# Kernel optimization log

Hardware: AMD Instinct MI355X
Metric: run time of the kernel (lower is better)

## Reference

```python
import jax, jax.numpy as jnp
import numpy as np

B, C_EDGE, C_FUSED, C_SEM = 4, 64, 128, 128
H = W = 64
MASK_SIZE = 11
EPS = 1e-6


def _window_mask(h, w, mask_size):
    # M_dw: 0 inside the clipped (mask_size x mask_size) window around each query pixel, -10000 outside.
    half = mask_size // 2
    idx = jnp.arange(h * w)
    qx, qy = idx // w, idx % w
    inside = (jnp.abs(qx[:, None] - qx[None, :]) <= half) & (jnp.abs(qy[:, None] - qy[None, :]) <= half)
    return jnp.where(inside, 0.0, -10000.0).astype(jnp.float32)


def _conv1x1(x, w, b):
    # x: [b, cin, h, w], w: [cout, cin]
    return jnp.einsum('bchw,oc->bohw', x, w) + b[None, :, None, None]


def _proj1d(x, w, b):
    # x: [b, cin, n], w: [cout, cin]
    return jnp.einsum('bcn,oc->bon', x, w) + b[None, :, None]


def _bilinear(x, h, w):
    # matches F.interpolate(mode='bilinear', align_corners=False)
    b, c = x.shape[0], x.shape[1]
    return jax.image.resize(x, (b, c, h, w), method='linear', antialias=False)


def setup_inputs() -> dict:
    key = jax.random.key(0)
    ks = jax.random.split(key, 13)
    s = 0.05
    return {
        'edge_features': jax.random.normal(ks[0], (B, C_EDGE, 32, 32), jnp.float32),
        'semantic_features': jax.random.normal(ks[1], (B, C_SEM, H, W), jnp.float32),
        'fused_features': jax.random.normal(ks[2], (B, C_FUSED, 32, 32), jnp.float32),
        'w_align': jax.random.normal(ks[3], (C_SEM, C_EDGE), jnp.float32) * s,
        'b_align': jax.random.normal(ks[4], (C_SEM,), jnp.float32) * s,
        'w_fused_align': jax.random.normal(ks[5], (C_SEM, C_FUSED), jnp.float32) * s,
        'b_fused_align': jax.random.normal(ks[6], (C_SEM,), jnp.float32) * s,
        'w_q': jax.random.normal(ks[7], (2 * C_SEM, 2 * C_SEM), jnp.float32) * s,
        'b_q': jax.random.normal(ks[8], (2 * C_SEM,), jnp.float32) * s,
        'w_k': jax.random.normal(ks[9], (2 * C_SEM, 2 * C_SEM), jnp.float32) * s,
        'b_k': jax.random.normal(ks[10], (2 * C_SEM,), jnp.float32) * s,
        'w_fusion': jax.random.normal(ks[11], (C_SEM, 2 * C_SEM), jnp.float32) * s,
        'b_fusion': jax.random.normal(ks[12], (C_SEM,), jnp.float32) * s,
    }


def reference(edge_features, semantic_features, fused_features,
              w_align, b_align, w_fused_align, b_fused_align,
              w_q, b_q, w_k, b_k, w_fusion, b_fusion):
    b, c, h, w = semantic_features.shape
    n = h * w

    edge = _conv1x1(_bilinear(edge_features, h, w), w_align, b_align)            # [b,c,h,w]
    fused = _conv1x1(_bilinear(fused_features, h, w), w_fused_align, b_fused_align)

    l2_edge = jnp.sqrt(jnp.sum(edge * edge, axis=1, keepdims=True))              # [b,1,h,w]
    l2_sem = jnp.sqrt(jnp.sum(semantic_features * semantic_features, axis=1, keepdims=True))
    similarity = jnp.sum((edge / (l2_edge + EPS)) * (semantic_features / (l2_sem + EPS)),
                         axis=1, keepdims=True)
    similarity = (similarity + 1.0) * 0.5

    density_flat = l2_edge.reshape(b, n)
    density = (jax.nn.softmax(density_flat, axis=1) * n).reshape(b, 1, h, w)

    edge_t = (edge * similarity).reshape(b, c, n)
    sem_t = (semantic_features * density).reshape(b, c, n)
    fused_t = fused.reshape(b, c, n)
    sem_raw = semantic_features.reshape(b, c, n)

    edge_cat = jnp.concatenate([edge_t, edge_t], axis=1)    # [b,2c,n]
    sem_cat = jnp.concatenate([sem_t, fused_t], axis=1)
    sem_val = jnp.concatenate([sem_raw, fused_t], axis=1)

    q = _proj1d(edge_cat, w_q, b_q)                          # [b,2c,n]
    k = _proj1d(sem_cat, w_k, b_k)

    scale = 1.0 / jnp.sqrt(jnp.float32(2 * c))
    attn = jnp.einsum('bcn,bcm->bnm', q, k) * scale          # [b,n,n]
    attn = attn + _window_mask(h, w, MASK_SIZE)
    attn = jax.nn.softmax(attn, axis=-1)

    out = jnp.einsum('bnm,bcm->bnc', attn, sem_val)          # [b,n,2c]
    out = out.reshape(b, h, w, 2 * c).transpose(0, 3, 1, 2)  # [b,2c,h,w]
    return _conv1x1(out, w_fusion, b_fusion)
```

## Files before the change

kernel.cpp:

```cpp
#include <hip/hip_runtime.h>
#include <hip/hip_bf16.h>

#define NB 4
#define C 128
#define N 4096
#define EPS 1e-6f
#define PW 80
#define PIMG 5120

typedef float f32x4 __attribute__((ext_vector_type(4)));
typedef short bf16x8 __attribute__((ext_vector_type(8)));
typedef unsigned short ushort_t;
typedef unsigned int uint_t;

__device__ __forceinline__ ushort_t f2bf(float f) {
  __hip_bfloat16 h = __float2bfloat16(f);
  return *reinterpret_cast<ushort_t*>(&h);
}

struct alignas(8) us4 { ushort_t a, b, c, d; };

__device__ __forceinline__ void conv_body(const float* __restrict__ x,
                                          const float* __restrict__ w,
                                          const float* __restrict__ bias,
                                          float* __restrict__ out,
                                          int n, int o0, int b, int CIN) {
  const float* xb = x + (size_t)(b * CIN) * 1024 + n;
  float a0 = 0.f, a1 = 0.f, a2 = 0.f, a3 = 0.f;
  for (int c = 0; c < CIN; ++c) {
    float xv = xb[(size_t)c * 1024];
    a0 += w[(o0 + 0) * CIN + c] * xv;
    a1 += w[(o0 + 1) * CIN + c] * xv;
    a2 += w[(o0 + 2) * CIN + c] * xv;
    a3 += w[(o0 + 3) * CIN + c] * xv;
  }
  size_t ob = ((size_t)b * 128 + o0) * 1024 + n;
  out[ob]        = a0 + bias[o0];
  out[ob + 1024] = a1 + bias[o0 + 1];
  out[ob + 2048] = a2 + bias[o0 + 2];
  out[ob + 3072] = a3 + bias[o0 + 3];
}

__global__ void prep_misc(const float* __restrict__ edge_f, const float* __restrict__ w_align,
                          const float* __restrict__ b_align,
                          const float* __restrict__ fused_f, const float* __restrict__ w_fal,
                          const float* __restrict__ b_fal,
                          const float* __restrict__ wq, const float* __restrict__ wk,
                          const float* __restrict__ wf,
                          ushort_t* __restrict__ wqf, ushort_t* __restrict__ wkf,
                          ushort_t* __restrict__ wff,
                          float* __restrict__ edge32, float* __restrict__ fused32,
                          float* __restrict__ dsum) {
  int bx = blockIdx.x, t = threadIdx.x;
  if (bx < 64) {
    if (bx == 0 && t < NB) dsum[t] = 0.f;
    int c = bx * 256 + t;
    int lane = c & 63;
    int mrow = lane & 15, quad = lane >> 4;
    if (c < 4096) {
      int grp = c >> 6;
      int tile = grp >> 2, kslot = grp & 3;
      int o = tile * 16 + mrow, k0 = kslot * 32 + quad * 8;
      const float* s = wq + o * 256 + k0;
      ushort_t* d = wqf + (size_t)c * 8;
#pragma unroll
      for (int j = 0; j < 8; ++j) d[j] = f2bf(s[j] + s[128 + j]);
    } else if (c < 12288) {
      int c2 = c - 4096;
      int grp = c2 >> 6;
      int tile = grp >> 3, kslot = grp & 7;
      int o = tile * 16 + mrow, k0 = kslot * 32 + quad * 8;
      const float* s = wk + o * 256 + k0;
      ushort_t* d = wkf + (size_t)c2 * 8;
#pragma unroll
      for (int j = 0; j < 8; ++j) d[j] = f2bf(s[j]);
    } else {
      int c2 = c - 12288;
      int grp = c2 >> 6;
      int tile = grp >> 3, kslot = grp & 7;
      int o = tile * 16 + mrow, k0 = kslot * 32 + quad * 8;
      const float* s = wf + o * 256 + k0;
      ushort_t* d = wff + (size_t)c2 * 8;
#pragma unroll
      for (int j = 0; j < 8; ++j) d[j] = f2bf(s[j]);
    }
  } else if (bx < 576) {
    int j = bx - 64;
    conv_body(edge_f, w_align, b_align, edge32, (j & 3) * 256 + t, ((j >> 2) & 31) * 4, j >> 7, 64);
  } else {
    int j = bx - 576;
    conv_body(fused_f, w_fal, b_fal, fused32, (j & 3) * 256 + t, ((j >> 2) & 31) * 4, j >> 7, 128);
  }
}

__global__ __launch_bounds__(512, 4) void prep_acts(const float* __restrict__ edge32,
                                                    const float* __restrict__ fused32,
                                                    const float* __restrict__ sem,
                                                    const ushort_t* __restrict__ wqf,
                                                    const ushort_t* __restrict__ wff,
                                                    const float* __restrict__ b_q,
                                                    ushort_t* __restrict__ xt_sem,
                                                    ushort_t* __restrict__ xt_fused,
                                                    float* __restrict__ simb,
                                                    float* __restrict__ l2e,
                                                    float* __restrict__ dsum,
                                                    ushort_t* __restrict__ qtb,
                                                    ushort_t* __restrict__ v2b) {
  int b = blockIdx.y, bx = blockIdx.x;
  int y = bx >> 1, xh = (bx & 1) * 32;
  int t = threadIdx.x;
  int nl = t & 31, cg = t >> 5;
  int x = xh + nl;
  int yy0 = (y & 1) ? (y >> 1) : (y >> 1) - 1;
  float fy = (y & 1) ? 0.25f : 0.75f;
  int y0c = max(yy0, 0), y1c = min(yy0 + 1, 31);
  int xx0 = (x & 1) ? (x >> 1) : (x >> 1) - 1;
  float fx = (x & 1) ? 0.25f : 0.75f;
  int x0c = max(xx0, 0), x1c = min(xx0 + 1, 31);

  __shared__ uint_t se[32][68], ssm[32][68], sf[32][68];
  __shared__ float red[8][3][32];
  __shared__ float simL[32];
  __shared__ ushort_t vstg[128 * 40];

  float ee = 0.f, ssum = 0.f, es = 0.f;
#pragma unroll 2
  for (int p = 0; p < 4; ++p) {
    float evs[2], fvs[2], svs[2];
#pragma unroll
    for (int u = 0; u < 2; ++u) {
      int c = cg * 8 + p * 2 + u;
      const float* ip = edge32 + ((size_t)(b * 128 + c)) * 1024;
      float e00 = ip[y0c * 32 + x0c], e01 = ip[y0c * 32 + x1c];
      float e10 = ip[y1c * 32 + x0c], e11 = ip[y1c * 32 + x1c];
      float ev = (1.f - fy) * ((1.f - fx) * e00 + fx * e01) + fy * ((1.f - fx) * e10 + fx * e11);
      const float* fp = fused32 + ((size_t)(b * 128 + c)) * 1024;
      float f00 = fp[y0c * 32 + x0c], f01 = fp[y0c * 32 + x1c];
      float f10 = fp[y1c * 32 + x0c], f11 = fp[y1c * 32 + x1c];
      float fv = (1.f - fy) * ((1.f - fx) * f00 + fx * f01) + fy * ((1.f - fx) * f10 + fx * f11);
      float sv = sem[((size_t)(b * 128 + c)) * 4096 + y * 64 + x];
      ee += ev * ev; ssum += sv * sv; es += ev * sv;
      evs[u] = ev; fvs[u] = fv; svs[u] = sv;
    }
    int col = cg * 4 + p;
    se[nl][col]  = (uint_t)f2bf(evs[0]) | ((uint_t)f2bf(evs[1]) << 16);
    sf[nl][col]  = (uint_t)f2bf(fvs[0]) | ((uint_t)f2bf(fvs[1]) << 16);
    ssm[nl][col] = (uint_t)f2bf(svs[0]) | ((uint_t)f2bf(svs[1]) << 16);
  }
  ee += __shfl_xor(ee, 32, 64); ssum += __shfl_xor(ssum, 32, 64); es += __shfl_xor(es, 32, 64);
  int w = t >> 6, lane = t & 63;
  int l15 = lane & 15, quad = lane >> 4;
  if (lane < 32) { red[w][0][lane] = ee; red[w][1][lane] = ssum; red[w][2][lane] = es; }
  __syncthreads();

  int base_n = b * 4096 + y * 64 + xh;
#pragma unroll
  for (int rep = 0; rep < 4; ++rep) {
    int d = rep * 512 + t;
    int r = d >> 6, cp = d & 63;
    ((uint_t*)xt_sem)[(size_t)(base_n + r) * 64 + cp] = ssm[r][cp];
    ((uint_t*)xt_fused)[(size_t)(base_n + r) * 64 + cp] = sf[r][cp];
  }
  if (t < 32) {
    float E = 0.f, S = 0.f, X = 0.f;
#pragma unroll
    for (int w2 = 0; w2 < 8; ++w2) { E += red[w2][0][t]; S += red[w2][1][t]; X += red[w2][2][t]; }
    float le = sqrtf(E), ls = sqrtf(S);
    float sv = (X / ((le + EPS) * (ls + EPS)) + 1.f) * 0.5f;
    simb[base_n + t] = sv;
    simL[t] = sv;
    l2e[base_n + t] = le;
    float pe = expf(le - 16.f);
#pragma unroll
    for (int m2 = 16; m2; m2 >>= 1) pe += __shfl_xor(pe, m2, 64);
    if (t == 0) atomicAdd(&dsum[b], pe);
  }
  __syncthreads();

#pragma unroll
  for (int h = 0; h < 2; ++h) {
    f32x4 vacc = (f32x4){0.f,0.f,0.f,0.f};
#pragma unroll
    for (int kk = 0; kk < 4; ++kk) {
      bf16x8 bfr = *(const bf16x8*)&ssm[h * 16 + l15][kk * 16 + quad * 4];
      bf16x8 afr = *(const bf16x8*)(wff + (size_t)((w * 8 + kk) * 64 + lane) * 8);
      vacc = __builtin_amdgcn_mfma_f32_16x16x32_bf16(afr, bfr, vacc, 0, 0, 0);
    }
#pragma unroll
    for (int kk = 0; kk < 4; ++kk) {
      bf16x8 bfr = *(const bf16x8*)&sf[h * 16 + l15][kk * 16 + quad * 4];
      bf16x8 afr = *(const bf16x8*)(wff + (size_t)((w * 8 + 4 + kk) * 64 + lane) * 8);
      vacc = __builtin_amdgcn_mfma_f32_16x16x32_bf16(afr, bfr, vacc, 0, 0, 0);
    }
#pragma unroll
    for (int r = 0; r < 4; ++r) {
      int ch = w * 16 + quad * 4 + r;
      vstg[ch * 40 + h * 16 + l15] = f2bf(vacc[r]);
    }
  }

#pragma unroll
  for (int h = 0; h < 2; ++h) {
    f32x4 qacc[2];
#pragma unroll
    for (int i = 0; i < 2; ++i) qacc[i] = (f32x4){0.f,0.f,0.f,0.f};
#pragma unroll
    for (int kk = 0; kk < 4; ++kk) {
      bf16x8 bfr = *(const bf16x8*)&se[h * 16 + l15][kk * 16 + quad * 4];
#pragma unroll
      for (int i = 0; i < 2; ++i) {
        bf16x8 afr = *(const bf16x8*)(wqf + (size_t)(((w * 2 + i) * 4 + kk) * 64 + lane) * 8);
        qacc[i] = __builtin_amdgcn_mfma_f32_16x16x32_bf16(afr, bfr, qacc[i], 0, 0, 0);
      }
    }
    int px = h * 16 + l15;
    float sv = simL[px];
    int n = y * 64 + xh + px;
#pragma unroll
    for (int i = 0; i < 2; ++i) {
      int o = (w * 2 + i) * 16 + quad * 4;
      float4 bq = *(const float4*)(b_q + o);
      us4 pk = { f2bf(sv * qacc[i][0] + bq.x), f2bf(sv * qacc[i][1] + bq.y),
                 f2bf(sv * qacc[i][2] + bq.z), f2bf(sv * qacc[i][3] + bq.w) };
      *(us4*)(qtb + ((size_t)b * N + n) * 256 + o) = pk;
    }
  }

  __syncthreads();
  int np0 = y * PW + 8 + xh;
  {
    int ch = t >> 2, seg = t & 3;
    *(bf16x8*)(v2b + ((size_t)b * 128 + ch) * PIMG + np0 + seg * 8) =
        *(const bf16x8*)&vstg[ch * 40 + seg * 8];
  }
}

__global__ __launch_bounds__(256, 4) void gemm_k(const ushort_t* __restrict__ xt_sem,
                                                 const ushort_t* __restrict__ xt_fused,
                                                 const ushort_t* __restrict__ wkf,
                                                 const float* __restrict__ b_k,
                                                 const float* __restrict__ l2e,
                                                 const float* __restrict__ dsum,
                                                 ushort_t* __restrict__ ktb) {
  int bx = blockIdx.x, bI = blockIdx.y;
  int t = threadIdx.x, w = t >> 6, lane = t & 63;
  int mrow = lane & 15, quad = lane >> 4;
  __shared__ __align__(16) ushort_t stg[16 * 264];

  int n0 = bx * 16, o0 = w * 64;
  float dscale = 4096.f / dsum[bI];
  const ushort_t* bS = xt_sem + ((size_t)bI * N + n0 + mrow) * 128 + quad * 8;
  const ushort_t* bF = xt_fused + ((size_t)bI * N + n0 + mrow) * 128 + quad * 8;
  f32x4 accL[4], accR[4];
#pragma unroll
  for (int i = 0; i < 4; ++i) { accL[i] = (f32x4){0.f,0.f,0.f,0.f}; accR[i] = (f32x4){0.f,0.f,0.f,0.f}; }
#pragma unroll
  for (int kk = 0; kk < 4; ++kk) {
    bf16x8 bfr = *(const bf16x8*)(bS + kk * 32);
#pragma unroll
    for (int i = 0; i < 4; ++i) {
      bf16x8 afr = *(const bf16x8*)(wkf + (size_t)((((w * 4 + i) * 8) + kk) * 64 + lane) * 8);
      accL[i] = __builtin_amdgcn_mfma_f32_16x16x32_bf16(afr, bfr, accL[i], 0, 0, 0);
    }
  }
#pragma unroll
  for (int kk = 0; kk < 4; ++kk) {
    bf16x8 bfr = *(const bf16x8*)(bF + kk * 32);
#pragma unroll
    for (int i = 0; i < 4; ++i) {
      bf16x8 afr = *(const bf16x8*)(wkf + (size_t)((((w * 4 + i) * 8) + 4 + kk) * 64 + lane) * 8);
      accR[i] = __builtin_amdgcn_mfma_f32_16x16x32_bf16(afr, bfr, accR[i], 0, 0, 0);
    }
  }
  int n = n0 + mrow;
  float dv = expf(l2e[bI * N + n] - 16.f) * dscale;
#pragma unroll
  for (int i = 0; i < 4; ++i) {
    int o = o0 + i * 16 + quad * 4;
    float4 bk = *(const float4*)(b_k + o);
    us4 pk = { f2bf(accL[i][0] * dv + accR[i][0] + bk.x),
               f2bf(accL[i][1] * dv + accR[i][1] + bk.y),
               f2bf(accL[i][2] * dv + accR[i][2] + bk.z),
               f2bf(accL[i][3] * dv + accR[i][3] + bk.w) };
    *(us4*)&stg[mrow * 264 + o] = pk;
  }
  __syncthreads();
  int np0 = (n0 >> 6) * PW + 8 + (n0 & 63);
#pragma unroll
  for (int r = 0; r < 2; ++r) {
    int cidx = r * 256 + t;
    int row = cidx >> 5, cc = cidx & 31;
    *(bf16x8*)(ktb + ((size_t)bI * PIMG + np0 + row) * 256 + cc * 8) =
        *(const bf16x8*)&stg[row * 264 + cc * 8];
  }
}

__global__ __launch_bounds__(256) void attn_kernel(const ushort_t* __restrict__ qtb,
                                                   const ushort_t* __restrict__ ktb,
                                                   const ushort_t* __restrict__ v2b,
                                                   const float* __restrict__ b_fusion,
                                                   float* __restrict__ out) {
  int L = blockIdx.x;
  int xcd = L & 7, j = L >> 3;
  int b = xcd >> 1;
  int ty0 = (((xcd & 1) << 3) + (j >> 3)) * 4;
  int tx0 = (j & 7) * 8;
  int y0 = max(ty0 - 5, 0), y1 = min(ty0 + 8, 63);
  int nh = y1 - y0 + 1;
  int x0a = tx0 - 8, cb = tx0;
  int ntq = (nh * 3 + 1) >> 1;
  int npv = (nh * 3 + 3) >> 2;

  __shared__ ushort_t pst[32][352];
  __shared__ float redm[4][2][16], reds[4][2][16];

  int t = threadIdx.x, w = t >> 6, lane = t & 63;
  int l15 = lane & 15, quad = lane >> 4;

  int gap = npv * 32 - ntq * 16;
  for (int idx = t; idx < 32 * gap; idx += 256)
    pst[idx & 31][ntq * 16 + (idx >> 5)] = 0;

  int n_s0 = (ty0 + (l15 >> 3)) * 64 + tx0 + (l15 & 7);
  int n_s1 = n_s0 + 128;
  bf16x8 qfr[2][8];
  {
    const ushort_t* q0 = qtb + ((size_t)b * N + n_s0) * 256 + quad * 8;
    const ushort_t* q1 = qtb + ((size_t)b * N + n_s1) * 256 + quad * 8;
#pragma unroll
    for (int ks = 0; ks < 8; ++ks) {
      qfr[0][ks] = *(const bf16x8*)(q0 + ks * 32);
      qfr[1][ks] = *(const bf16x8*)(q1 + ks * 32);
    }
  }
  int qx = tx0 + (l15 & 7);
  int qy0 = ty0 + (l15 >> 3);

  const ushort_t* kb = ktb + (size_t)b * PIMG * 256;
  f32x4 sc[6][2];
#pragma unroll
  for (int i = 0; i < 6; ++i) {
    int tq = w + i * 4;
    if (tq >= ntq) break;
    int key = tq * 16 + l15;
    int ry = (key * 2731) >> 16;
    int rx = key - ry * 24;
    int yy = min(y0 + ry, 63);
    const ushort_t* krow = kb + (size_t)(yy * PW + cb + rx) * 256 + quad * 8;
    f32x4 a0 = (f32x4){0.f,0.f,0.f,0.f}, a1 = (f32x4){0.f,0.f,0.f,0.f};
#pragma unroll
    for (int ks = 0; ks < 8; ++ks) {
      bf16x8 afr = *(const bf16x8*)(krow + ks * 32);
      a0 = __builtin_amdgcn_mfma_f32_16x16x32_bf16(afr, qfr[0][ks], a0, 0, 0, 0);
      a1 = __builtin_amdgcn_mfma_f32_16x16x32_bf16(afr, qfr[1][ks], a1, 0, 0, 0);
    }
    sc[i][0] = a0; sc[i][1] = a1;
  }
  float mymax0 = -1e30f, mymax1 = -1e30f;
#pragma unroll
  for (int i = 0; i < 6; ++i) {
    int tq = w + i * 4;
    if (tq >= ntq) break;
#pragma unroll
    for (int r = 0; r < 4; ++r) {
      int key = tq * 16 + quad * 4 + r;
      int ry = (key * 2731) >> 16;
      int rx = key - ry * 24;
      int x = x0a + rx;
      int dx = x - qx;
      bool xok = (dx >= -5) && (dx <= 5) && (x >= 0) && (x <= 63) && (ry < nh);
      int dy0 = y0 + ry - qy0;
      float s0 = (xok && dy0 >= -5 && dy0 <= 5) ? sc[i][0][r] * 0.0625f : -1e30f;
      int dy1 = dy0 - 2;
      float s1 = (xok && dy1 >= -5 && dy1 <= 5) ? sc[i][1][r] * 0.0625f : -1e30f;
      sc[i][0][r] = s0; sc[i][1][r] = s1;
      mymax0 = fmaxf(mymax0, s0); mymax1 = fmaxf(mymax1, s1);
    }
  }
  mymax0 = fmaxf(mymax0, __shfl_xor(mymax0, 16, 64));
  mymax0 = fmaxf(mymax0, __shfl_xor(mymax0, 32, 64));
  mymax1 = fmaxf(mymax1, __shfl_xor(mymax1, 16, 64));
  mymax1 = fmaxf(mymax1, __shfl_xor(mymax1, 32, 64));
  if (quad == 0) { redm[w][0][l15] = mymax0; redm[w][1][l15] = mymax1; }
  __syncthreads();
  float gmax0 = fmaxf(fmaxf(redm[0][0][l15], redm[1][0][l15]), fmaxf(redm[2][0][l15], redm[3][0][l15]));
  float gmax1 = fmaxf(fmaxf(redm[0][1][l15], redm[1][1][l15]), fmaxf(redm[2][1][l15], redm[3][1][l15]));
  float mysum0 = 0.f, mysum1 = 0.f;
#pragma unroll
  for (int i = 0; i < 6; ++i) {
    int tq = w + i * 4;
    if (tq >= ntq) break;
#pragma unroll
    for (int r = 0; r < 4; ++r) {
      float e0 = expf(sc[i][0][r] - gmax0);
      float e1 = expf(sc[i][1][r] - gmax1);
      sc[i][0][r] = e0; sc[i][1][r] = e1;
      mysum0 += e0; mysum1 += e1;
    }
  }
  mysum0 += __shfl_xor(mysum0, 16, 64); mysum0 += __shfl_xor(mysum0, 32, 64);
  mysum1 += __shfl_xor(mysum1, 16, 64); mysum1 += __shfl_xor(mysum1, 32, 64);
  if (quad == 0) { reds[w][0][l15] = mysum0; reds[w][1][l15] = mysum1; }
#pragma unroll
  for (int i = 0; i < 6; ++i) {
    int tq = w + i * 4;
    if (tq >= ntq) break;
    int kc = tq * 16 + quad * 4;
#pragma unroll
    for (int s = 0; s < 2; ++s) {
      uint_t p01 = (uint_t)f2bf(sc[i][s][0]) | ((uint_t)f2bf(sc[i][s][1]) << 16);
      uint_t p23 = (uint_t)f2bf(sc[i][s][2]) | ((uint_t)f2bf(sc[i][s][3]) << 16);
      *(uint_t*)(&pst[s * 16 + l15][kc]) = p01;
      *(uint_t*)(&pst[s * 16 + l15][kc + 2]) = p23;
    }
  }
  __syncthreads();

  float rinv0 = 1.f / (reds[0][0][l15] + reds[1][0][l15] + reds[2][0][l15] + reds[3][0][l15]);
  float rinv1 = 1.f / (reds[0][1][l15] + reds[1][1][l15] + reds[2][1][l15] + reds[3][1][l15]);

  const ushort_t* vb = v2b + (size_t)b * 128 * PIMG;
#pragma unroll
  for (int half = 0; half < 2; ++half) {
    int ch0 = half * 64 + w * 16;
    const ushort_t* vrow = vb + (size_t)(ch0 + l15) * PIMG;
    f32x4 acc0 = (f32x4){0.f,0.f,0.f,0.f}, acc1 = (f32x4){0.f,0.f,0.f,0.f};
    for (int ks = 0; ks < npv; ++ks) {
      int kst = ks * 32 + quad * 8;
      int ry = (kst * 2731) >> 16;
      int rxs = kst - ry * 24;
      int yy = min(y0 + ry, 63);
      bf16x8 av = *(const bf16x8*)(vrow + yy * PW + cb + rxs);
      bf16x8 bp0 = *(const bf16x8*)(&pst[l15][kst]);
      bf16x8 bp1 = *(const bf16x8*)(&pst[16 + l15][kst]);
      acc0 = __builtin_amdgcn_mfma_f32_16x16x32_bf16(av, bp0, acc0, 0, 0, 0);
      acc1 = __builtin_amdgcn_mfma_f32_16x16x32_bf16(av, bp1, acc1, 0, 0, 0);
    }
    int chg = ch0 + quad * 4;
    float4 bf4 = *(const float4*)(b_fusion + chg);
    float bfa[4] = {bf4.x, bf4.y, bf4.z, bf4.w};
#pragma unroll
    for (int r = 0; r < 4; ++r) {
      out[((size_t)b * 128 + chg + r) * N + n_s0] = acc0[r] * rinv0 + bfa[r];
      out[((size_t)b * 128 + chg + r) * N + n_s1] = acc1[r] * rinv1 + bfa[r];
    }
  }
}

extern "C" void kernel_launch(void* const* d_in, const int* in_sizes, int n_in,
                              void* d_out, int out_size, void* d_ws, size_t ws_size,
                              hipStream_t stream) {
  (void)in_sizes; (void)n_in; (void)out_size; (void)ws_size;
  const float* edge_f  = (const float*)d_in[0];
  const float* sem     = (const float*)d_in[1];
  const float* fused_f = (const float*)d_in[2];
  const float* w_align = (const float*)d_in[3];
  const float* b_align = (const float*)d_in[4];
  const float* w_fal   = (const float*)d_in[5];
  const float* b_fal   = (const float*)d_in[6];
  const float* w_q     = (const float*)d_in[7];
  const float* b_q     = (const float*)d_in[8];
  const float* w_k     = (const float*)d_in[9];
  const float* b_k     = (const float*)d_in[10];
  const float* w_fus   = (const float*)d_in[11];
  const float* b_fus   = (const float*)d_in[12];
  float* out = (float*)d_out;

  float* ws = (float*)d_ws;
  float* edge32   = ws;
  float* fused32  = ws + 524288;
  float* simb     = ws + 1048576;
  float* l2e      = ws + 1064960;
  float* dsum     = ws + 1081344;
  ushort_t* xt_sem   = (ushort_t*)(ws + 1097728);
  ushort_t* xt_fused = (ushort_t*)(ws + 2146304);
  ushort_t* wqf      = (ushort_t*)(ws + 3194880);
  ushort_t* wkf      = (ushort_t*)(ws + 3211264);
  ushort_t* wff      = (ushort_t*)(ws + 3244032);
  ushort_t* qtb      = (ushort_t*)(ws + 3260416);
  ushort_t* ktb      = (ushort_t*)(ws + 5357568);
  ushort_t* v2b      = (ushort_t*)(ws + 7979008);

  prep_misc<<<1088, 256, 0, stream>>>(edge_f, w_align, b_align, fused_f, w_fal, b_fal,
                                      w_q, w_k, w_fus, wqf, wkf, wff, edge32, fused32, dsum);
  prep_acts<<<dim3(128, NB), 512, 0, stream>>>(edge32, fused32, sem, wqf, wff, b_q,
                                               xt_sem, xt_fused, simb, l2e, dsum, qtb, v2b);
  gemm_k<<<dim3(256, NB), 256, 0, stream>>>(xt_sem, xt_fused, wkf, b_k, l2e, dsum, ktb);
  attn_kernel<<<512, 256, 0, stream>>>(qtb, ktb, v2b, b_fus, out);
}
```

Baseline: 159.6 us.

## Fuse K projection into prep_acts via cooperative grid sync

```diff
diff --git a/kernel.cpp b/kernel.cpp
--- a/kernel.cpp
+++ b/kernel.cpp
@@ -1,5 +1,8 @@
 #include <hip/hip_runtime.h>
 #include <hip/hip_bf16.h>
+#include <hip/hip_cooperative_groups.h>
+
+namespace cgrp = cooperative_groups;
 
 #define NB 4
 #define C 128
@@ -93,205 +96,192 @@
   }
 }
 
-__global__ __launch_bounds__(512, 4) void prep_acts(const float* __restrict__ edge32,
+__global__ __launch_bounds__(512, 2) void prep_acts(const float* __restrict__ edge32,
                                                     const float* __restrict__ fused32,
                                                     const float* __restrict__ sem,
                                                     const ushort_t* __restrict__ wqf,
+                                                    const ushort_t* __restrict__ wkf,
                                                     const ushort_t* __restrict__ wff,
                                                     const float* __restrict__ b_q,
-                                                    ushort_t* __restrict__ xt_sem,
-                                                    ushort_t* __restrict__ xt_fused,
-                                                    float* __restrict__ simb,
-                                                    float* __restrict__ l2e,
+                                                    const float* __restrict__ b_k,
                                                     float* __restrict__ dsum,
                                                     ushort_t* __restrict__ qtb,
+                                                    ushort_t* __restrict__ ktb,
                                                     ushort_t* __restrict__ v2b) {
-  int b = blockIdx.y, bx = blockIdx.x;
-  int y = bx >> 1, xh = (bx & 1) * 32;
+  __shared__ uint_t se[2][32][68], ssm[2][32][68], sf[2][32][68];
+  __shared__ float red[8][3][32];
+  __shared__ float simL[2][32], l2eL[2][32];
+  __shared__ ushort_t vstg[128 * 40];
+  __shared__ __align__(16) ushort_t kstg[32 * 264];
+
   int t = threadIdx.x;
-  int nl = t & 31, cg = t >> 5;
-  int x = xh + nl;
-  int yy0 = (y & 1) ? (y >> 1) : (y >> 1) - 1;
-  float fy = (y & 1) ? 0.25f : 0.75f;
-  int y0c = max(yy0, 0), y1c = min(yy0 + 1, 31);
-  int xx0 = (x & 1) ? (x >> 1) : (x >> 1) - 1;
-  float fx = (x & 1) ? 0.25f : 0.75f;
-  int x0c = max(xx0, 0), x1c = min(xx0 + 1, 31);
-
-  __shared__ uint_t se[32][68], ssm[32][68], sf[32][68];
-  __shared__ float red[8][3][32];
-  __shared__ float simL[32];
-  __shared__ ushort_t vstg[128 * 40];
-
-  float ee = 0.f, ssum = 0.f, es = 0.f;
-#pragma unroll 2
-  for (int p = 0; p < 4; ++p) {
-    float evs[2], fvs[2], svs[2];
-#pragma unroll
-    for (int u = 0; u < 2; ++u) {
-      int c = cg * 8 + p * 2 + u;
-      const float* ip = edge32 + ((size_t)(b * 128 + c)) * 1024;
-      float e00 = ip[y0c * 32 + x0c], e01 = ip[y0c * 32 + x1c];
-      float e10 = ip[y1c * 32 + x0c], e11 = ip[y1c * 32 + x1c];
-      float ev = (1.f - fy) * ((1.f - fx) * e00 + fx * e01) + fy * ((1.f - fx) * e10 + fx * e11);
-      const float* fp = fused32 + ((size_t)(b * 128 + c)) * 1024;
-      float f00 = fp[y0c * 32 + x0c], f01 = fp[y0c * 32 + x1c];
-      float f10 = fp[y1c * 32 + x0c], f11 = fp[y1c * 32 + x1c];
-      float fv = (1.f - fy) * ((1.f - fx) * f00 + fx * f01) + fy * ((1.f - fx) * f10 + fx * f11);
-      float sv = sem[((size_t)(b * 128 + c)) * 4096 + y * 64 + x];
-      ee += ev * ev; ssum += sv * sv; es += ev * sv;
-      evs[u] = ev; fvs[u] = fv; svs[u] = sv;
-    }
-    int col = cg * 4 + p;
-    se[nl][col]  = (uint_t)f2bf(evs[0]) | ((uint_t)f2bf(evs[1]) << 16);
-    sf[nl][col]  = (uint_t)f2bf(fvs[0]) | ((uint_t)f2bf(fvs[1]) << 16);
-    ssm[nl][col] = (uint_t)f2bf(svs[0]) | ((uint_t)f2bf(svs[1]) << 16);
-  }
-  ee += __shfl_xor(ee, 32, 64); ssum += __shfl_xor(ssum, 32, 64); es += __shfl_xor(es, 32, 64);
+  int nl = t & 31, cgi = t >> 5;
   int w = t >> 6, lane = t & 63;
   int l15 = lane & 15, quad = lane >> 4;
-  if (lane < 32) { red[w][0][lane] = ee; red[w][1][lane] = ssum; red[w][2][lane] = es; }
-  __syncthreads();
-
-  int base_n = b * 4096 + y * 64 + xh;
-#pragma unroll
-  for (int rep = 0; rep < 4; ++rep) {
-    int d = rep * 512 + t;
-    int r = d >> 6, cp = d & 63;
-    ((uint_t*)xt_sem)[(size_t)(base_n + r) * 64 + cp] = ssm[r][cp];
-    ((uint_t*)xt_fused)[(size_t)(base_n + r) * 64 + cp] = sf[r][cp];
-  }
-  if (t < 32) {
-    float E = 0.f, S = 0.f, X = 0.f;
-#pragma unroll
-    for (int w2 = 0; w2 < 8; ++w2) { E += red[w2][0][t]; S += red[w2][1][t]; X += red[w2][2][t]; }
-    float le = sqrtf(E), ls = sqrtf(S);
-    float sv = (X / ((le + EPS) * (ls + EPS)) + 1.f) * 0.5f;
-    simb[base_n + t] = sv;
-    simL[t] = sv;
-    l2e[base_n + t] = le;
-    float pe = expf(le - 16.f);
-#pragma unroll
-    for (int m2 = 16; m2; m2 >>= 1) pe += __shfl_xor(pe, m2, 64);
-    if (t == 0) atomicAdd(&dsum[b], pe);
-  }
-  __syncthreads();
-
-#pragma unroll
-  for (int h = 0; h < 2; ++h) {
-    f32x4 vacc = (f32x4){0.f,0.f,0.f,0.f};
-#pragma unroll
-    for (int kk = 0; kk < 4; ++kk) {
-      bf16x8 bfr = *(const bf16x8*)&ssm[h * 16 + l15][kk * 16 + quad * 4];
-      bf16x8 afr = *(const bf16x8*)(wff + (size_t)((w * 8 + kk) * 64 + lane) * 8);
-      vacc = __builtin_amdgcn_mfma_f32_16x16x32_bf16(afr, bfr, vacc, 0, 0, 0);
-    }
-#pragma unroll
-    for (int kk = 0; kk < 4; ++kk) {
-      bf16x8 bfr = *(const bf16x8*)&sf[h * 16 + l15][kk * 16 + quad * 4];
-      bf16x8 afr = *(const bf16x8*)(wff + (size_t)((w * 8 + 4 + kk) * 64 + lane) * 8);
-      vacc = __builtin_amdgcn_mfma_f32_16x16x32_bf16(afr, bfr, vacc, 0, 0, 0);
-    }
-#pragma unroll
-    for (int r = 0; r < 4; ++r) {
-      int ch = w * 16 + quad * 4 + r;
-      vstg[ch * 40 + h * 16 + l15] = f2bf(vacc[r]);
-    }
-  }
-
-#pragma unroll
-  for (int h = 0; h < 2; ++h) {
-    f32x4 qacc[2];
-#pragma unroll
-    for (int i = 0; i < 2; ++i) qacc[i] = (f32x4){0.f,0.f,0.f,0.f};
-#pragma unroll
-    for (int kk = 0; kk < 4; ++kk) {
-      bf16x8 bfr = *(const bf16x8*)&se[h * 16 + l15][kk * 16 + quad * 4];
+
+  for (int u = 0; u < 2; ++u) {
+    int L = (int)blockIdx.x + u * 256;
+    int b = L >> 7, bxu = L & 127;
+    int y = bxu >> 1, xh = (bxu & 1) * 32;
+    int x = xh + nl;
+    int yy0 = (y & 1) ? (y >> 1) : (y >> 1) - 1;
+    float fy = (y & 1) ? 0.25f : 0.75f;
+    int y0c = max(yy0, 0), y1c = min(yy0 + 1, 31);
+    int xx0 = (x & 1) ? (x >> 1) : (x >> 1) - 1;
+    float fx = (x & 1) ? 0.25f : 0.75f;
+    int x0c = max(xx0, 0), x1c = min(xx0 + 1, 31);
+
+    float ee = 0.f, ssum = 0.f, es = 0.f;
+#pragma unroll 2
+    for (int p = 0; p < 4; ++p) {
+      float evs[2], fvs[2], svs[2];
+#pragma unroll
+      for (int uu = 0; uu < 2; ++uu) {
+        int c = cgi * 8 + p * 2 + uu;
+        const float* ip = edge32 + ((size_t)(b * 128 + c)) * 1024;
+        float e00 = ip[y0c * 32 + x0c], e01 = ip[y0c * 32 + x1c];
+        float e10 = ip[y1c * 32 + x0c], e11 = ip[y1c * 32 + x1c];
+        float ev = (1.f - fy) * ((1.f - fx) * e00 + fx * e01) + fy * ((1.f - fx) * e10 + fx * e11);
+        const float* fp = fused32 + ((size_t)(b * 128 + c)) * 1024;
+        float f00 = fp[y0c * 32 + x0c], f01 = fp[y0c * 32 + x1c];
+        float f10 = fp[y1c * 32 + x0c], f11 = fp[y1c * 32 + x1c];
+        float fv = (1.f - fy) * ((1.f - fx) * f00 + fx * f01) + fy * ((1.f - fx) * f10 + fx * f11);
+        float sv = sem[((size_t)(b * 128 + c)) * 4096 + y * 64 + x];
+        ee += ev * ev; ssum += sv * sv; es += ev * sv;
+        evs[uu] = ev; fvs[uu] = fv; svs[uu] = sv;
+      }
+      int col = cgi * 4 + p;
+      se[u][nl][col]  = (uint_t)f2bf(evs[0]) | ((uint_t)f2bf(evs[1]) << 16);
+      sf[u][nl][col]  = (uint_t)f2bf(fvs[0]) | ((uint_t)f2bf(fvs[1]) << 16);
+      ssm[u][nl][col] = (uint_t)f2bf(svs[0]) | ((uint_t)f2bf(svs[1]) << 16);
+    }
+    ee += __shfl_xor(ee, 32, 64); ssum += __shfl_xor(ssum, 32, 64); es += __shfl_xor(es, 32, 64);
+    if (lane < 32) { red[w][0][lane] = ee; red[w][1][lane] = ssum; red[w][2][lane] = es; }
+    __syncthreads();
+    if (t < 32) {
+      float E = 0.f, S = 0.f, X = 0.f;
+#pragma unroll
+      for (int w2 = 0; w2 < 8; ++w2) { E += red[w2][0][t]; S += red[w2][1][t]; X += red[w2][2][t]; }
+      float le = sqrtf(E), ls = sqrtf(S);
+      float sv = (X / ((le + EPS) * (ls + EPS)) + 1.f) * 0.5f;
+      simL[u][t] = sv;
+      l2eL[u][t] = le;
+      float pe = expf(le - 16.f);
+#pragma unroll
+      for (int m2 = 16; m2; m2 >>= 1) pe += __shfl_xor(pe, m2, 64);
+      if (t == 0) atomicAdd(&dsum[b], pe);
+    }
+    __syncthreads();
+  }
+
+  cgrp::this_grid().sync();
+
+  for (int u = 0; u < 2; ++u) {
+    int L = (int)blockIdx.x + u * 256;
+    int b = L >> 7, bxu = L & 127;
+    int y = bxu >> 1, xh = (bxu & 1) * 32;
+    int np0 = y * PW + 8 + xh;
+    float dscale = 4096.f / __hip_atomic_load(&dsum[b], __ATOMIC_RELAXED, __HIP_MEMORY_SCOPE_AGENT);
+
+#pragma unroll
+    for (int h = 0; h < 2; ++h) {
+      f32x4 vacc = (f32x4){0.f,0.f,0.f,0.f};
+#pragma unroll
+      for (int kk = 0; kk < 4; ++kk) {
+        bf16x8 bfr = *(const bf16x8*)&ssm[u][h * 16 + l15][kk * 16 + quad * 4];
+        bf16x8 afr = *(const bf16x8*)(wff + (size_t)((w * 8 + kk) * 64 + lane) * 8);
+        vacc = __builtin_amdgcn_mfma_f32_16x16x32_bf16(afr, bfr, vacc, 0, 0, 0);
+      }
+#pragma unroll
+      for (int kk = 0; kk < 4; ++kk) {
+        bf16x8 bfr = *(const bf16x8*)&sf[u][h * 16 + l15][kk * 16 + quad * 4];
+        bf16x8 afr = *(const bf16x8*)(wff + (size_t)((w * 8 + 4 + kk) * 64 + lane) * 8);
+        vacc = __builtin_amdgcn_mfma_f32_16x16x32_bf16(afr, bfr, vacc, 0, 0, 0);
+      }
+#pragma unroll
+      for (int r = 0; r < 4; ++r) {
+        int ch = w * 16 + quad * 4 + r;
+        vstg[ch * 40 + h * 16 + l15] = f2bf(vacc[r]);
+      }
+    }
+    __syncthreads();
+    {
+      int ch = t >> 2, seg = t & 3;
+      *(bf16x8*)(v2b + ((size_t)b * 128 + ch) * PIMG + np0 + seg * 8) =
+          *(const bf16x8*)&vstg[ch * 40 + seg * 8];
+    }
+
+#pragma unroll
+    for (int h = 0; h < 2; ++h) {
+      f32x4 aL[2], aR[2];
+#pragma unroll
+      for (int i = 0; i < 2; ++i) { aL[i] = (f32x4){0.f,0.f,0.f,0.f}; aR[i] = (f32x4){0.f,0.f,0.f,0.f}; }
+#pragma unroll
+      for (int kk = 0; kk < 4; ++kk) {
+        bf16x8 bfr = *(const bf16x8*)&ssm[u][h * 16 + l15][kk * 16 + quad * 4];
+#pragma unroll
+        for (int i = 0; i < 2; ++i) {
+          bf16x8 afr = *(const bf16x8*)(wkf + (size_t)((((w * 2 + i) * 8) + kk) * 64 + lane) * 8);
+          aL[i] = __builtin_amdgcn_mfma_f32_16x16x32_bf16(afr, bfr, aL[i], 0, 0, 0);
+        }
+      }
+#pragma unroll
+      for (int kk = 0; kk < 4; ++kk) {
+        bf16x8 bfr = *(const bf16x8*)&sf[u][h * 16 + l15][kk * 16 + quad * 4];
+#pragma unroll
+        for (int i = 0; i < 2; ++i) {
+          bf16x8 afr = *(const bf16x8*)(wkf + (size_t)((((w * 2 + i) * 8) + 4 + kk) * 64 + lane) * 8);
+          aR[i] = __builtin_amdgcn_mfma_f32_16x16x32_bf16(afr, bfr, aR[i], 0, 0, 0);
+        }
+      }
+      float dv = expf(l2eL[u][h * 16 + l15] - 16.f) * dscale;
 #pragma unroll
       for (int i = 0; i < 2; ++i) {
-        bf16x8 afr = *(const bf16x8*)(wqf + (size_t)(((w * 2 + i) * 4 + kk) * 64 + lane) * 8);
-        qacc[i] = __builtin_amdgcn_mfma_f32_16x16x32_bf16(afr, bfr, qacc[i], 0, 0, 0);
-      }
-    }
-    int px = h * 16 + l15;
-    float sv = simL[px];
-    int n = y * 64 + xh + px;
-#pragma unroll
-    for (int i = 0; i < 2; ++i) {
-      int o = (w * 2 + i) * 16 + quad * 4;
-      float4 bq = *(const float4*)(b_q + o);
-      us4 pk = { f2bf(sv * qacc[i][0] + bq.x), f2bf(sv * qacc[i][1] + bq.y),
-                 f2bf(sv * qacc[i][2] + bq.z), f2bf(sv * qacc[i][3] + bq.w) };
-      *(us4*)(qtb + ((size_t)b * N + n) * 256 + o) = pk;
-    }
-  }
-
-  __syncthreads();
-  int np0 = y * PW + 8 + xh;
-  {
-    int ch = t >> 2, seg = t & 3;
-    *(bf16x8*)(v2b + ((size_t)b * 128 + ch) * PIMG + np0 + seg * 8) =
-        *(const bf16x8*)&vstg[ch * 40 + seg * 8];
-  }
-}
-
-__global__ __launch_bounds__(256, 4) void gemm_k(const ushort_t* __restrict__ xt_sem,
-                                                 const ushort_t* __restrict__ xt_fused,
-                                                 const ushort_t* __restrict__ wkf,
-                                                 const float* __restrict__ b_k,
-                                                 const float* __restrict__ l2e,
-                                                 const float* __restrict__ dsum,
-                                                 ushort_t* __restrict__ ktb) {
-  int bx = blockIdx.x, bI = blockIdx.y;
-  int t = threadIdx.x, w = t >> 6, lane = t & 63;
-  int mrow = lane & 15, quad = lane >> 4;
-  __shared__ __align__(16) ushort_t stg[16 * 264];
-
-  int n0 = bx * 16, o0 = w * 64;
-  float dscale = 4096.f / dsum[bI];
-  const ushort_t* bS = xt_sem + ((size_t)bI * N + n0 + mrow) * 128 + quad * 8;
-  const ushort_t* bF = xt_fused + ((size_t)bI * N + n0 + mrow) * 128 + quad * 8;
-  f32x4 accL[4], accR[4];
-#pragma unroll
-  for (int i = 0; i < 4; ++i) { accL[i] = (f32x4){0.f,0.f,0.f,0.f}; accR[i] = (f32x4){0.f,0.f,0.f,0.f}; }
-#pragma unroll
-  for (int kk = 0; kk < 4; ++kk) {
-    bf16x8 bfr = *(const bf16x8*)(bS + kk * 32);
-#pragma unroll
-    for (int i = 0; i < 4; ++i) {
-      bf16x8 afr = *(const bf16x8*)(wkf + (size_t)((((w * 4 + i) * 8) + kk) * 64 + lane) * 8);
-      accL[i] = __builtin_amdgcn_mfma_f32_16x16x32_bf16(afr, bfr, accL[i], 0, 0, 0);
-    }
-  }
-#pragma unroll
-  for (int kk = 0; kk < 4; ++kk) {
-    bf16x8 bfr = *(const bf16x8*)(bF + kk * 32);
-#pragma unroll
-    for (int i = 0; i < 4; ++i) {
-      bf16x8 afr = *(const bf16x8*)(wkf + (size_t)((((w * 4 + i) * 8) + 4 + kk) * 64 + lane) * 8);
-      accR[i] = __builtin_amdgcn_mfma_f32_16x16x32_bf16(afr, bfr, accR[i], 0, 0, 0);
-    }
-  }
-  int n = n0 + mrow;
-  float dv = expf(l2e[bI * N + n] - 16.f) * dscale;
-#pragma unroll
-  for (int i = 0; i < 4; ++i) {
-    int o = o0 + i * 16 + quad * 4;
-    float4 bk = *(const float4*)(b_k + o);
-    us4 pk = { f2bf(accL[i][0] * dv + accR[i][0] + bk.x),
-               f2bf(accL[i][1] * dv + accR[i][1] + bk.y),
-               f2bf(accL[i][2] * dv + accR[i][2] + bk.z),
-               f2bf(accL[i][3] * dv + accR[i][3] + bk.w) };
-    *(us4*)&stg[mrow * 264 + o] = pk;
-  }
-  __syncthreads();
-  int np0 = (n0 >> 6) * PW + 8 + (n0 & 63);
-#pragma unroll
-  for (int r = 0; r < 2; ++r) {
-    int cidx = r * 256 + t;
-    int row = cidx >> 5, cc = cidx & 31;
-    *(bf16x8*)(ktb + ((size_t)bI * PIMG + np0 + row) * 256 + cc * 8) =
-        *(const bf16x8*)&stg[row * 264 + cc * 8];
+        int o = (w * 2 + i) * 16 + quad * 4;
+        float4 bk4 = *(const float4*)(b_k + o);
+        us4 pk = { f2bf(aL[i][0] * dv + aR[i][0] + bk4.x),
+                   f2bf(aL[i][1] * dv + aR[i][1] + bk4.y),
+                   f2bf(aL[i][2] * dv + aR[i][2] + bk4.z),
+                   f2bf(aL[i][3] * dv + aR[i][3] + bk4.w) };
+        *(us4*)&kstg[(h * 16 + l15) * 264 + o] = pk;
+      }
+    }
+    __syncthreads();
+#pragma unroll
+    for (int r = 0; r < 2; ++r) {
+      int idx = r * 512 + t;
+      int row = idx >> 5, cc = idx & 31;
+      *(bf16x8*)(ktb + ((size_t)b * PIMG + np0 + row) * 256 + cc * 8) =
+          *(const bf16x8*)&kstg[row * 264 + cc * 8];
+    }
+
+#pragma unroll
+    for (int h = 0; h < 2; ++h) {
+      f32x4 qacc[2];
+#pragma unroll
+      for (int i = 0; i < 2; ++i) qacc[i] = (f32x4){0.f,0.f,0.f,0.f};
+#pragma unroll
+      for (int kk = 0; kk < 4; ++kk) {
+        bf16x8 bfr = *(const bf16x8*)&se[u][h * 16 + l15][kk * 16 + quad * 4];
+#pragma unroll
+        for (int i = 0; i < 2; ++i) {
+          bf16x8 afr = *(const bf16x8*)(wqf + (size_t)(((w * 2 + i) * 4 + kk) * 64 + lane) * 8);
+          qacc[i] = __builtin_amdgcn_mfma_f32_16x16x32_bf16(afr, bfr, qacc[i], 0, 0, 0);
+        }
+      }
+      int px = h * 16 + l15;
+      float sv = simL[u][px];
+      int n = y * 64 + xh + px;
+#pragma unroll
+      for (int i = 0; i < 2; ++i) {
+        int o = (w * 2 + i) * 16 + quad * 4;
+        float4 bq = *(const float4*)(b_q + o);
+        us4 pk = { f2bf(sv * qacc[i][0] + bq.x), f2bf(sv * qacc[i][1] + bq.y),
+                   f2bf(sv * qacc[i][2] + bq.z), f2bf(sv * qacc[i][3] + bq.w) };
+        *(us4*)(qtb + ((size_t)b * N + n) * 256 + o) = pk;
+      }
+    }
+    __syncthreads();
   }
 }
 
@@ -469,11 +459,7 @@
   float* ws = (float*)d_ws;
   float* edge32   = ws;
   float* fused32  = ws + 524288;
-  float* simb     = ws + 1048576;
-  float* l2e      = ws + 1064960;
   float* dsum     = ws + 1081344;
-  ushort_t* xt_sem   = (ushort_t*)(ws + 1097728);
-  ushort_t* xt_fused = (ushort_t*)(ws + 2146304);
   ushort_t* wqf      = (ushort_t*)(ws + 3194880);
   ushort_t* wkf      = (ushort_t*)(ws + 3211264);
   ushort_t* wff      = (ushort_t*)(ws + 3244032);
@@ -483,8 +469,13 @@
 
   prep_misc<<<1088, 256, 0, stream>>>(edge_f, w_align, b_align, fused_f, w_fal, b_fal,
                                       w_q, w_k, w_fus, wqf, wkf, wff, edge32, fused32, dsum);
-  prep_acts<<<dim3(128, NB), 512, 0, stream>>>(edge32, fused32, sem, wqf, wff, b_q,
-                                               xt_sem, xt_fused, simb, l2e, dsum, qtb, v2b);
-  gemm_k<<<dim3(256, NB), 256, 0, stream>>>(xt_sem, xt_fused, wkf, b_k, l2e, dsum, ktb);
+
+  void* pa_args[] = { (void*)&edge32, (void*)&fused32, (void*)&sem,
+                      (void*)&wqf, (void*)&wkf, (void*)&wff,
+                      (void*)&b_q, (void*)&b_k, (void*)&dsum,
+                      (void*)&qtb, (void*)&ktb, (void*)&v2b };
+  hipLaunchCooperativeKernel(reinterpret_cast<void*>(&prep_acts),
+                             dim3(256), dim3(512), pa_args, 0, stream);
+
   attn_kernel<<<512, 256, 0, stream>>>(qtb, ktb, v2b, b_fus, out);
 }
```

Result: slower. 205.7 us (+28.9%).
